# Kernel tuning notes

Hardware: AMD Instinct MI355X
Metric: run time of the kernel (lower is better)

Reference implementation:

```python
import jax, jax.numpy as jnp
import numpy as np

B, IN_DIM, HID, LAT, L, K = 65536, 512, 256, 64, 3, 2048


def setup_inputs() -> dict:
    key = jax.random.key(0)
    ks = jax.random.split(key, 10)
    s = 0.05
    return {
        "x": jax.random.normal(ks[0], (B, IN_DIM), jnp.float32),
        "enc_w1": jax.random.normal(ks[1], (IN_DIM, HID), jnp.float32) * s,
        "enc_b1": jnp.zeros((HID,), jnp.float32),
        "enc_w2": jax.random.normal(ks[2], (HID, LAT), jnp.float32) * s,
        "enc_b2": jnp.zeros((LAT,), jnp.float32),
        "codebooks": jax.random.normal(ks[3], (L, K, LAT), jnp.float32),
        "dec_w1": jax.random.normal(ks[4], (LAT, HID), jnp.float32) * s,
        "dec_b1": jnp.zeros((HID,), jnp.float32),
        "dec_w2": jax.random.normal(ks[5], (HID, IN_DIM), jnp.float32) * s,
        "dec_b2": jnp.zeros((IN_DIM,), jnp.float32),
    }


def reference(x, enc_w1, enc_b1, enc_w2, enc_b2, codebooks,
              dec_w1, dec_b1, dec_w2, dec_b2):
    # encoder: Linear -> ReLU -> Linear
    z = jax.nn.relu(x @ enc_w1 + enc_b1) @ enc_w2 + enc_b2  # [B, LAT]

    quantized = jnp.zeros_like(z)
    codes, residuals = [], []
    num_layers = codebooks.shape[0]
    for i in range(num_layers):  # small fixed layer loop (structurally sequential)
        residual = z - jax.lax.stop_gradient(quantized)  # [B, LAT]
        residuals.append(residual)
        C = codebooks[i]  # [K, LAT]
        # squared euclidean distances (argmin identical to cdist argmin)
        sqdist = (jnp.sum(residual * residual, axis=-1, keepdims=True)
                  - 2.0 * (residual @ C.T)
                  + jnp.sum(C * C, axis=-1))  # [B, K]
        code = jnp.argmin(sqdist, axis=-1)  # [B]
        codes.append(code)
        quantized = C[code] + jax.lax.stop_gradient(quantized)

    # decoder: Linear -> ReLU -> Linear
    x_recon = jax.nn.relu(quantized @ dec_w1 + dec_b1) @ dec_w2 + dec_b2  # [B, IN_DIM]
    return (jnp.stack(codes), x_recon, quantized, jnp.stack(residuals))
```

## Files before the change

### kernel.cpp

```cpp
#include <hip/hip_runtime.h>
#include <float.h>

#define NB      65536
#define IN_DIM  512
#define HID     256
#define LAT     64
#define NLAYERS 3
#define NK      2048
#define DELTA   1e-2f

typedef __attribute__((ext_vector_type(8)))  short s16x8;
typedef __attribute__((ext_vector_type(16))) float fp32x16;

__device__ __forceinline__ unsigned short f2bf(float v) {
  unsigned u = __float_as_uint(v);
  unsigned r = (u + 0x7fffu + ((u >> 16) & 1u)) >> 16;
  return (unsigned short)r;
}
__device__ __forceinline__ float bf2f(unsigned short h) {
  return __uint_as_float((unsigned)h << 16);
}

template<bool RELU>
__global__ __launch_bounds__(256) void gemm_f32(
    const float* __restrict__ A, const float* __restrict__ W,
    const float* __restrict__ bias, float* __restrict__ C,
    int M, int N, int K) {
  __shared__ float As[32][132];
  __shared__ float Bs[32][64];
  const int tid = threadIdx.x;
  const int cg  = tid & 15;
  const int rg  = tid >> 4;
  const int m0  = blockIdx.x * 128;
  const int n0  = blockIdx.y * 64;

  float acc[8][4];
#pragma unroll
  for (int i = 0; i < 8; ++i)
#pragma unroll
    for (int j = 0; j < 4; ++j) acc[i][j] = 0.f;

  for (int k0 = 0; k0 < K; k0 += 32) {
#pragma unroll
    for (int p = 0; p < 4; ++p) {
      int a = tid + p * 256;
      int row = a >> 3, kq = (a & 7) * 4;
      float4 v = *reinterpret_cast<const float4*>(&A[(size_t)(m0 + row) * K + k0 + kq]);
      As[kq + 0][row] = v.x; As[kq + 1][row] = v.y;
      As[kq + 2][row] = v.z; As[kq + 3][row] = v.w;
    }
#pragma unroll
    for (int p = 0; p < 2; ++p) {
      int a = tid + p * 256;
      int kk = a >> 4, nq = (a & 15) * 4;
      *reinterpret_cast<float4*>(&Bs[kk][nq]) =
          *reinterpret_cast<const float4*>(&W[(size_t)(k0 + kk) * N + n0 + nq]);
    }
    __syncthreads();
#pragma unroll
    for (int kk = 0; kk < 32; ++kk) {
      float4 a0 = *reinterpret_cast<const float4*>(&As[kk][rg * 8]);
      float4 a1 = *reinterpret_cast<const float4*>(&As[kk][rg * 8 + 4]);
      float4 b0 = *reinterpret_cast<const float4*>(&Bs[kk][cg * 4]);
      float av[8] = {a0.x, a0.y, a0.z, a0.w, a1.x, a1.y, a1.z, a1.w};
      float bv[4] = {b0.x, b0.y, b0.z, b0.w};
#pragma unroll
      for (int i = 0; i < 8; ++i)
#pragma unroll
        for (int j = 0; j < 4; ++j)
          acc[i][j] = fmaf(av[i], bv[j], acc[i][j]);
    }
    __syncthreads();
  }

  float4 bb = *reinterpret_cast<const float4*>(&bias[n0 + cg * 4]);
  float bv[4] = {bb.x, bb.y, bb.z, bb.w};
#pragma unroll
  for (int i = 0; i < 8; ++i) {
    float vals[4];
#pragma unroll
    for (int j = 0; j < 4; ++j) {
      float v = __fadd_rn(acc[i][j], bv[j]);
      if (RELU) v = fmaxf(v, 0.f);
      vals[j] = v;
    }
    float4 o; o.x = vals[0]; o.y = vals[1]; o.z = vals[2]; o.w = vals[3];
    *reinterpret_cast<float4*>(&C[(size_t)(m0 + rg * 8 + i) * N + n0 + cg * 4]) = o;
  }
}

template<bool RELU>
__global__ __launch_bounds__(256) void gemm128(
    const float* __restrict__ A, const float* __restrict__ W,
    const float* __restrict__ bias, float* __restrict__ C,
    int M, int N, int K) {
  __shared__ float As[16][132];
  __shared__ float Bs[16][132];
  const int tid  = threadIdx.x;
  const int cg   = tid & 15;
  const int rg   = tid >> 4;
  const int sw   = (cg >> 2) & 1;
  const int colA = cg * 8 + sw * 4;
  const int colB = cg * 8 + (sw ^ 1) * 4;
  const int m0   = blockIdx.x * 128;
  const int n0   = blockIdx.y * 128;

  const int arow = tid >> 2;
  const int akq  = (tid & 3) * 4;
  const int bk   = tid >> 5;
  const int bn   = (tid & 31) * 4;

  const float* Ap0 = A + (size_t)(m0 + arow) * K + akq;
  const float* Ap1 = A + (size_t)(m0 + arow + 64) * K + akq;
  const float* Wp0 = W + (size_t)bk * N + n0 + bn;
  const float* Wp1 = W + (size_t)(bk + 8) * N + n0 + bn;

  float acc[8][8];
#pragma unroll
  for (int i = 0; i < 8; ++i)
#pragma unroll
    for (int j = 0; j < 8; ++j) acc[i][j] = 0.f;

  float4 av0, av1, bv0, bv1;
  av0 = *reinterpret_cast<const float4*>(Ap0);
  av1 = *reinterpret_cast<const float4*>(Ap1);
  bv0 = *reinterpret_cast<const float4*>(Wp0);
  bv1 = *reinterpret_cast<const float4*>(Wp1);

  auto write_tile = [&]() {
    As[akq + 0][arow] = av0.x; As[akq + 1][arow] = av0.y;
    As[akq + 2][arow] = av0.z; As[akq + 3][arow] = av0.w;
    As[akq + 0][arow + 64] = av1.x; As[akq + 1][arow + 64] = av1.y;
    As[akq + 2][arow + 64] = av1.z; As[akq + 3][arow + 64] = av1.w;
    *reinterpret_cast<float4*>(&Bs[bk][bn])     = bv0;
    *reinterpret_cast<float4*>(&Bs[bk + 8][bn]) = bv1;
  };
  auto compute_tile = [&]() {
#pragma unroll
    for (int kk = 0; kk < 16; ++kk) {
      float4 a0 = *reinterpret_cast<const float4*>(&As[kk][rg * 8]);
      float4 a1 = *reinterpret_cast<const float4*>(&As[kk][rg * 8 + 4]);
      float4 b0 = *reinterpret_cast<const float4*>(&Bs[kk][colA]);
      float4 b1 = *reinterpret_cast<const float4*>(&Bs[kk][colB]);
      float rv[8] = {a0.x, a0.y, a0.z, a0.w, a1.x, a1.y, a1.z, a1.w};
      float cv[8] = {b0.x, b0.y, b0.z, b0.w, b1.x, b1.y, b1.z, b1.w};
#pragma unroll
      for (int i = 0; i < 8; ++i)
#pragma unroll
        for (int j = 0; j < 8; ++j)
          acc[i][j] = fmaf(rv[i], cv[j], acc[i][j]);
    }
  };

  write_tile();
  __syncthreads();
#pragma unroll 1
  for (int k0 = 16; k0 < K; k0 += 16) {
    av0 = *reinterpret_cast<const float4*>(Ap0 + k0);
    av1 = *reinterpret_cast<const float4*>(Ap1 + k0);
    bv0 = *reinterpret_cast<const float4*>(Wp0 + (size_t)k0 * N);
    bv1 = *reinterpret_cast<const float4*>(Wp1 + (size_t)k0 * N);
    compute_tile();
    __syncthreads();
    write_tile();
    __syncthreads();
  }
  compute_tile();

  float4 bA = *reinterpret_cast<const float4*>(&bias[n0 + colA]);
  float4 bB = *reinterpret_cast<const float4*>(&bias[n0 + colB]);
  float ba[8] = {bA.x, bA.y, bA.z, bA.w, bB.x, bB.y, bB.z, bB.w};
#pragma unroll
  for (int i = 0; i < 8; ++i) {
    size_t row = (size_t)(m0 + rg * 8 + i);
    float o[8];
#pragma unroll
    for (int j = 0; j < 8; ++j) {
      float v = __fadd_rn(acc[i][j], ba[j]);
      if (RELU) v = fmaxf(v, 0.f);
      o[j] = v;
    }
    float4 oA; oA.x = o[0]; oA.y = o[1]; oA.z = o[2]; oA.w = o[3];
    float4 oB; oB.x = o[4]; oB.y = o[5]; oB.z = o[6]; oB.w = o[7];
    *reinterpret_cast<float4*>(&C[row * N + n0 + colA]) = oA;
    *reinterpret_cast<float4*>(&C[row * N + n0 + colB]) = oB;
  }
}

__global__ void cnorm_f32(const float* __restrict__ cb, float* __restrict__ cn) {
  int i = blockIdx.x * blockDim.x + threadIdx.x;
  if (i >= NLAYERS * NK) return;
  const float* row = cb + (size_t)i * LAT;
  float r[8];
#pragma unroll
  for (int j = 0; j < 8; ++j) r[j] = 0.f;
#pragma unroll
  for (int t = 0; t < 8; ++t)
#pragma unroll
    for (int j = 0; j < 8; ++j) {
      float v = row[t * 8 + j];
      r[j] = __fadd_rn(r[j], __fmul_rn(v, v));
    }
  cn[i] = __fadd_rn(__fadd_rn(__fadd_rn(r[0], r[1]), __fadd_rn(r[2], r[3])),
                    __fadd_rn(__fadd_rn(r[4], r[5]), __fadd_rn(r[6], r[7])));
}

__global__ void split_cb(const float* __restrict__ cb,
                         unsigned short* __restrict__ cbf) {
  const int sid  = blockIdx.x * 256 + threadIdx.x;
  const int lane = sid & 63;
  const int grp  = sid >> 6;
  const int fg   = grp & 7;
  const int chl  = grp >> 3;
  const int nt = fg >> 2, ks = fg & 3;
  const int layer = chl >> 5, ch = chl & 31;
  const int code = ch * 64 + nt * 32 + (lane & 31);
  const int k0 = ks * 16 + (lane >> 5) * 8;
  const float* src = cb + ((size_t)layer * NK + code) * LAT + k0;
  float4 a = *(const float4*)src;
  float4 b = *(const float4*)(src + 4);
  float v[8] = {a.x, a.y, a.z, a.w, b.x, b.y, b.z, b.w};
  s16x8 hi, lo;
#pragma unroll
  for (int i = 0; i < 8; ++i) {
    unsigned short h = f2bf(v[i]);
    hi[i] = (short)h;
    lo[i] = (short)f2bf(__fsub_rn(v[i], bf2f(h)));
  }
  *(s16x8*)(cbf + ((size_t)grp * 2 + 0) * 512 + lane * 8) = hi;
  *(s16x8*)(cbf + ((size_t)grp * 2 + 1) * 512 + lane * 8) = lo;
}

__global__ __launch_bounds__(256, 2) void rq_mfma(
    const float* __restrict__ zg,
    const float* __restrict__ cb,
    const unsigned short* __restrict__ cbf,
    const float* __restrict__ cnorm,
    float* __restrict__ out_codes,
    float* __restrict__ out_quant,
    float* __restrict__ out_res) {
  __shared__ float m1S[128][2];
  __shared__ int   candS[128][8];
  __shared__ int   cntS[128][2];
  __shared__ int   flagS[128][2];
  __shared__ int   selS[128];
  __shared__ float rnS[128];
  __shared__ float bestD[256];
  __shared__ int   bestK[256];

  const int tid   = threadIdx.x;
  const int w     = tid >> 6;
  const int rgrp  = w >> 1;
  const int chalf = w & 1;
  const int lane  = tid & 63;
  const int half  = lane >> 5;
  const int lcol  = lane & 31;
  const int rb0   = blockIdx.x * 128;

  s16x8 ah[2][4], al[2][4];

  for (int layer = 0; layer < NLAYERS; ++layer) {
    const float* cbL = cb + (size_t)layer * NK * LAT;
    const float* cnL = cnorm + (size_t)layer * NK;
    const unsigned short* cbfL = cbf + (size_t)layer * (NK * LAT * 2);
    float* resL = out_res + (size_t)layer * NB * LAT;

#pragma unroll
    for (int m = 0; m < 2; ++m) {
      const size_t row = (size_t)(rb0 + rgrp * 64 + m * 32 + lcol);
#pragma unroll
      for (int ks = 0; ks < 4; ++ks) {
        const int k0 = ks * 16 + half * 8;
        const float* zp = zg + row * LAT + k0;
        float4 a = *(const float4*)zp;
        float4 b = *(const float4*)(zp + 4);
        float r[8] = {a.x, a.y, a.z, a.w, b.x, b.y, b.z, b.w};
        if (layer > 0) {
          const float* qp = out_quant + row * LAT + k0;
          float4 qa = *(const float4*)qp;
          float4 qb = *(const float4*)(qp + 4);
          float q[8] = {qa.x, qa.y, qa.z, qa.w, qb.x, qb.y, qb.z, qb.w};
#pragma unroll
          for (int i = 0; i < 8; ++i) r[i] = __fsub_rn(r[i], q[i]);
          if (chalf == 0) {
            float4 o0 = {r[0], r[1], r[2], r[3]};
            float4 o1 = {r[4], r[5], r[6], r[7]};
            *(float4*)(resL + row * LAT + k0) = o0;
            *(float4*)(resL + row * LAT + k0 + 4) = o1;
          }
        }
#pragma unroll
        for (int i = 0; i < 8; ++i) {
          unsigned short hh = f2bf(r[i]);
          float hf = bf2f(hh);
          ah[m][ks][i] = (short)hh;
          al[m][ks][i] = (short)f2bf(__fsub_rn(r[i], hf));
        }
      }
    }
    __syncthreads();

    if (tid < 128) {
      const float* rp = resL + (size_t)(rb0 + tid) * LAT;
      float r8[8] = {0.f, 0.f, 0.f, 0.f, 0.f, 0.f, 0.f, 0.f};
#pragma unroll
      for (int tb = 0; tb < 8; ++tb) {
        float4 x0 = *(const float4*)(rp + tb * 8);
        float4 x1 = *(const float4*)(rp + tb * 8 + 4);
        float v[8] = {x0.x, x0.y, x0.z, x0.w, x1.x, x1.y, x1.z, x1.w};
#pragma unroll
        for (int j = 0; j < 8; ++j)
          r8[j] = __fadd_rn(r8[j], __fmul_rn(v[j], v[j]));
      }
      rnS[tid] = __fadd_rn(
          __fadd_rn(__fadd_rn(r8[0], r8[1]), __fadd_rn(r8[2], r8[3])),
          __fadd_rn(__fadd_rn(r8[4], r8[5]), __fadd_rn(r8[6], r8[7])));
    }

    float v1[2][16], v2[2][16];
    int   i1[2][16];
#pragma unroll
    for (int m = 0; m < 2; ++m)
#pragma unroll
      for (int r = 0; r < 16; ++r) {
        v1[m][r] = FLT_MAX; v2[m][r] = FLT_MAX; i1[m][r] = 0;
      }

#pragma unroll 1
    for (int ch = 0; ch < 16; ++ch) {
      const int chg = chalf * 16 + ch;
      const unsigned short* cf = cbfL + (size_t)chg * 8192;
#pragma unroll
      for (int nt = 0; nt < 2; ++nt) {
        const int kbase = chg * 64 + nt * 32 + lcol;
        float cnv = cnL[kbase];
        s16x8 bh[4], bl[4];
#pragma unroll
        for (int ks = 0; ks < 4; ++ks) {
          bh[ks] = *(const s16x8*)(cf + ((size_t)((nt * 4 + ks) * 2 + 0) * 64 + lane) * 8);
          bl[ks] = *(const s16x8*)(cf + ((size_t)((nt * 4 + ks) * 2 + 1) * 64 + lane) * 8);
        }
        fp32x16 acc0, acc1;
#pragma unroll
        for (int r = 0; r < 16; ++r) { acc0[r] = 0.f; acc1[r] = 0.f; }
#pragma unroll
        for (int ks = 0; ks < 4; ++ks) {
          acc0 = __builtin_amdgcn_mfma_f32_32x32x16_bf16(ah[0][ks], bh[ks], acc0, 0, 0, 0);
          acc1 = __builtin_amdgcn_mfma_f32_32x32x16_bf16(ah[1][ks], bh[ks], acc1, 0, 0, 0);
          acc0 = __builtin_amdgcn_mfma_f32_32x32x16_bf16(ah[0][ks], bl[ks], acc0, 0, 0, 0);
          acc1 = __builtin_amdgcn_mfma_f32_32x32x16_bf16(ah[1][ks], bl[ks], acc1, 0, 0, 0);
          acc0 = __builtin_amdgcn_mfma_f32_32x32x16_bf16(al[0][ks], bh[ks], acc0, 0, 0, 0);
          acc1 = __builtin_amdgcn_mfma_f32_32x32x16_bf16(al[1][ks], bh[ks], acc1, 0, 0, 0);
        }
#pragma unroll
        for (int r = 0; r < 16; ++r) {
          float d0 = fmaf(-2.f, acc0[r], cnv);
          bool c0 = d0 < v1[0][r];
          v2[0][r] = c0 ? v1[0][r] : fminf(v2[0][r], d0);
          v1[0][r] = c0 ? d0 : v1[0][r];
          i1[0][r] = c0 ? kbase : i1[0][r];
          float d1 = fmaf(-2.f, acc1[r], cnv);
          bool c1 = d1 < v1[1][r];
          v2[1][r] = c1 ? v1[1][r] : fminf(v2[1][r], d1);
          v1[1][r] = c1 ? d1 : v1[1][r];
          i1[1][r] = c1 ? kbase : i1[1][r];
        }
      }
    }

#pragma unroll
    for (int m = 0; m < 2; ++m)
#pragma unroll
      for (int r = 0; r < 16; ++r) {
        float m1 = v1[m][r];
        m1 = fminf(m1, __shfl_xor(m1, 1));
        m1 = fminf(m1, __shfl_xor(m1, 2));
        m1 = fminf(m1, __shfl_xor(m1, 4));
        m1 = fminf(m1, __shfl_xor(m1, 8));
        m1 = fminf(m1, __shfl_xor(m1, 16));
        const int rowloc = rgrp * 64 + m * 32 + (r & 3) + 8 * (r >> 2) + 4 * half;
        if (lcol == 0) m1S[rowloc][chalf] = m1;
      }
    __syncthreads();
#pragma unroll
    for (int m = 0; m < 2; ++m)
#pragma unroll
      for (int r = 0; r < 16; ++r) {
        const int rowloc = rgrp * 64 + m * 32 + (r & 3) + 8 * (r >> 2) + 4 * half;
        float thr = fminf(m1S[rowloc][0], m1S[rowloc][1]) + DELTA;
        unsigned long long bc = __ballot(v1[m][r] <= thr);
        unsigned long long bf = __ballot(v2[m][r] <= thr);
        unsigned mc = (unsigned)(bc >> (half * 32));
        unsigned mf = (unsigned)(bf >> (half * 32));
        int pos = __popc(mc & ((1u << lcol) - 1u));
        if (v1[m][r] <= thr && pos < 4) candS[rowloc][chalf * 4 + pos] = i1[m][r];
        if (lcol == 0) {
          int c = __popc(mc);
          cntS[rowloc][chalf]  = (c < 4) ? c : 4;
          flagS[rowloc][chalf] = (mf != 0u) || (c > 4);
        }
      }
    __syncthreads();

    if (tid < 128) {
      const int t = tid;
      if ((flagS[t][0] | flagS[t][1]) == 0) {
        const float* rp = resL + (size_t)(rb0 + t) * LAT;
        float rr[64];
#pragma unroll
        for (int j = 0; j < 16; ++j) {
          float4 x = *(const float4*)(rp + j * 4);
          rr[j * 4 + 0] = x.x; rr[j * 4 + 1] = x.y;
          rr[j * 4 + 2] = x.z; rr[j * 4 + 3] = x.w;
        }
        const float rn = rnS[t];
        float bd = FLT_MAX; int bk = 0x7fffffff;
        const int c0 = cntS[t][0], c1n = cntS[t][1];
        for (int c = 0; c < c0 + c1n; ++c) {
          int k = candS[t][(c < c0) ? c : (4 + c - c0)];
          const float* cp = cbL + (size_t)k * LAT;
          float dot = 0.f;
#pragma unroll
          for (int j = 0; j < 64; ++j) dot = fmaf(rr[j], cp[j], dot);
          float d = __fadd_rn(__fsub_rn(rn, __fmul_rn(2.f, dot)), cnL[k]);
          if (d < bd || (d == bd && k < bk)) { bd = d; bk = k; }
        }
        selS[t] = bk;
        out_codes[(size_t)layer * NB + rb0 + t] = (float)bk;
      }
    }
    __syncthreads();

#pragma unroll 1
    for (int t2 = 0; t2 < 128; ++t2) {
      if ((flagS[t2][0] | flagS[t2][1]) == 0) continue;
      const float* rp = resL + (size_t)(rb0 + t2) * LAT;
      const float rn = rnS[t2];
      float bd = FLT_MAX; int bk = 0x7fffffff;
#pragma unroll 1
      for (int j = 0; j < 8; ++j) {
        int k = tid * 8 + j;
        const float* cp = cbL + (size_t)k * LAT;
        float dot = 0.f;
        for (int q = 0; q < 64; ++q) dot = fmaf(rp[q], cp[q], dot);
        float d = __fadd_rn(__fsub_rn(rn, __fmul_rn(2.f, dot)), cnL[k]);
        if (d < bd || (d == bd && k < bk)) { bd = d; bk = k; }
      }
      bestD[tid] = bd; bestK[tid] = bk;
      __syncthreads();
      if (tid == 0) {
        float gd = FLT_MAX; int gk = 0x7fffffff;
        for (int i = 0; i < 256; ++i) {
          float d = bestD[i]; int k = bestK[i];
          if (d < gd || (d == gd && k < gk)) { gd = d; gk = k; }
        }
        selS[t2] = gk;
        out_codes[(size_t)layer * NB + rb0 + t2] = (float)gk;
      }
      __syncthreads();
    }

    if (chalf == 0) {
#pragma unroll
      for (int m = 0; m < 2; ++m) {
        const int rowloc = rgrp * 64 + m * 32 + lcol;
        const size_t row = (size_t)(rb0 + rowloc);
        const int sel = selS[rowloc];
        const float* cp = cbL + (size_t)sel * LAT;
#pragma unroll
        for (int ks = 0; ks < 4; ++ks) {
          const int k0 = ks * 16 + half * 8;
          float4 c0 = *(const float4*)(cp + k0);
          float4 c1 = *(const float4*)(cp + k0 + 4);
          float* qp = out_quant + row * LAT + k0;
          if (layer == 0) {
            *(float4*)qp = c0; *(float4*)(qp + 4) = c1;
          } else {
            float4 q0 = *(const float4*)qp;
            float4 q1 = *(const float4*)(qp + 4);
            q0.x = __fadd_rn(c0.x, q0.x); q0.y = __fadd_rn(c0.y, q0.y);
            q0.z = __fadd_rn(c0.z, q0.z); q0.w = __fadd_rn(c0.w, q0.w);
            q1.x = __fadd_rn(c1.x, q1.x); q1.y = __fadd_rn(c1.y, q1.y);
            q1.z = __fadd_rn(c1.z, q1.z); q1.w = __fadd_rn(c1.w, q1.w);
            *(float4*)qp = q0; *(float4*)(qp + 4) = q1;
          }
        }
      }
    }
    __syncthreads();
  }
}

extern "C" void kernel_launch(void* const* d_in, const int* in_sizes, int n_in,
                              void* d_out, int out_size, void* d_ws, size_t ws_size,
                              hipStream_t stream) {
  (void)in_sizes; (void)n_in; (void)out_size; (void)ws_size;
  const float* x   = (const float*)d_in[0];
  const float* ew1 = (const float*)d_in[1];
  const float* eb1 = (const float*)d_in[2];
  const float* ew2 = (const float*)d_in[3];
  const float* eb2 = (const float*)d_in[4];
  const float* cbk = (const float*)d_in[5];
  const float* dw1 = (const float*)d_in[6];
  const float* db1 = (const float*)d_in[7];
  const float* dw2 = (const float*)d_in[8];
  const float* db2 = (const float*)d_in[9];

  float* out     = (float*)d_out;
  float* o_codes = out;
  float* o_xrec  = out + (size_t)NLAYERS * NB;
  float* o_quant = o_xrec + (size_t)NB * IN_DIM;
  float* o_res   = o_quant + (size_t)NB * LAT;

  float* h  = (float*)d_ws;
  float* cn = h + (size_t)NB * HID;
  unsigned short* cbf = (unsigned short*)(o_xrec + (size_t)16 * 1024 * 1024);

  cnorm_f32<<<(NLAYERS * NK + 255) / 256, 256, 0, stream>>>(cbk, cn);
  split_cb<<<192, 256, 0, stream>>>(cbk, cbf);
  gemm128<true ><<<dim3(NB / 128, HID / 128),    256, 0, stream>>>(x, ew1, eb1, h,     NB, HID,    IN_DIM);
  gemm_f32<false><<<dim3(NB / 128, LAT / 64),    256, 0, stream>>>(h, ew2, eb2, o_res, NB, LAT,    HID);
  rq_mfma<<<NB / 128, 256, 0, stream>>>(o_res, cbk, cbf, cn, o_codes, o_quant, o_res);
  gemm128<true ><<<dim3(NB / 128, HID / 128),    256, 0, stream>>>(o_quant, dw1, db1, h,      NB, HID,    LAT);
  gemm128<false><<<dim3(NB / 128, IN_DIM / 128), 256, 0, stream>>>(h,       dw2, db2, o_xrec, NB, IN_DIM, HID);
}
```

Before: 825.2 us.

## Use split-bf16 MFMA decoder GEMMs and split RQ codebook scan across four waves

Adds split_w to pre-split the decoder weights into bf16 hi/lo MFMA fragments. It replaces the decoder's FP32 gemm128 calls with dec1/dec2 kernels that use 3-pass bf16 MFMA, storing the hidden activations as bf16 hi/lo pairs. The RQ kernel now handles 64 rows per block, with each of the four waves scanning a quarter of the codebook, which doubles the grid. The top-2 update is rewritten with min/max instead of selects. The split-bf16 path adds error versus FP32 and depends on the workspace being large enough, otherwise it falls back to the old path.

```diff
diff --git a/kernel.cpp b/kernel.cpp
--- a/kernel.cpp
+++ b/kernel.cpp
@@ -231,6 +231,30 @@
   *(s16x8*)(cbf + ((size_t)grp * 2 + 1) * 512 + lane * 8) = lo;
 }
 
+__global__ void split_w(const float* __restrict__ W,
+                        unsigned short* __restrict__ wf, int K, int N) {
+  const int total = (K / 16) * (N / 32) * 64;
+  const int idx = blockIdx.x * 256 + threadIdx.x;
+  if (idx >= total) return;
+  const int lane = idx & 63;
+  const int grp  = idx >> 6;
+  const int ntn  = N / 32;
+  const int ks   = grp / ntn;
+  const int ntg  = grp % ntn;
+  const int col  = ntg * 32 + (lane & 31);
+  const int k0   = ks * 16 + (lane >> 5) * 8;
+  s16x8 hi, lo;
+#pragma unroll
+  for (int i = 0; i < 8; ++i) {
+    float v = W[(size_t)(k0 + i) * N + col];
+    unsigned short h = f2bf(v);
+    hi[i] = (short)h;
+    lo[i] = (short)f2bf(__fsub_rn(v, bf2f(h)));
+  }
+  *(s16x8*)(wf + ((size_t)grp * 2 + 0) * 512 + lane * 8) = hi;
+  *(s16x8*)(wf + ((size_t)grp * 2 + 1) * 512 + lane * 8) = lo;
+}
+
 __global__ __launch_bounds__(256, 2) void rq_mfma(
     const float* __restrict__ zg,
     const float* __restrict__ cb,
@@ -239,23 +263,21 @@
     float* __restrict__ out_codes,
     float* __restrict__ out_quant,
     float* __restrict__ out_res) {
-  __shared__ float m1S[128][2];
-  __shared__ int   candS[128][8];
-  __shared__ int   cntS[128][2];
-  __shared__ int   flagS[128][2];
-  __shared__ int   selS[128];
-  __shared__ float rnS[128];
+  __shared__ float m1S[64][4];
+  __shared__ int   candS[64][16];
+  __shared__ int   cntS[64][4];
+  __shared__ int   flagS[64][4];
+  __shared__ int   selS[64];
+  __shared__ float rnS[64];
   __shared__ float bestD[256];
   __shared__ int   bestK[256];
 
-  const int tid   = threadIdx.x;
-  const int w     = tid >> 6;
-  const int rgrp  = w >> 1;
-  const int chalf = w & 1;
-  const int lane  = tid & 63;
-  const int half  = lane >> 5;
-  const int lcol  = lane & 31;
-  const int rb0   = blockIdx.x * 128;
+  const int tid  = threadIdx.x;
+  const int w    = tid >> 6;
+  const int lane = tid & 63;
+  const int half = lane >> 5;
+  const int lcol = lane & 31;
+  const int rb0  = blockIdx.x * 64;
 
   s16x8 ah[2][4], al[2][4];
 
@@ -267,7 +289,7 @@
 
 #pragma unroll
     for (int m = 0; m < 2; ++m) {
-      const size_t row = (size_t)(rb0 + rgrp * 64 + m * 32 + lcol);
+      const size_t row = (size_t)(rb0 + m * 32 + lcol);
 #pragma unroll
       for (int ks = 0; ks < 4; ++ks) {
         const int k0 = ks * 16 + half * 8;
@@ -282,7 +304,7 @@
           float q[8] = {qa.x, qa.y, qa.z, qa.w, qb.x, qb.y, qb.z, qb.w};
 #pragma unroll
           for (int i = 0; i < 8; ++i) r[i] = __fsub_rn(r[i], q[i]);
-          if (chalf == 0) {
+          if (w == 0) {
             float4 o0 = {r[0], r[1], r[2], r[3]};
             float4 o1 = {r[4], r[5], r[6], r[7]};
             *(float4*)(resL + row * LAT + k0) = o0;
@@ -300,7 +322,7 @@
     }
     __syncthreads();
 
-    if (tid < 128) {
+    if (tid < 64) {
       const float* rp = resL + (size_t)(rb0 + tid) * LAT;
       float r8[8] = {0.f, 0.f, 0.f, 0.f, 0.f, 0.f, 0.f, 0.f};
 #pragma unroll
@@ -327,8 +349,8 @@
       }
 
 #pragma unroll 1
-    for (int ch = 0; ch < 16; ++ch) {
-      const int chg = chalf * 16 + ch;
+    for (int ch = 0; ch < 8; ++ch) {
+      const int chg = w * 8 + ch;
       const unsigned short* cf = cbfL + (size_t)chg * 8192;
 #pragma unroll
       for (int nt = 0; nt < 2; ++nt) {
@@ -354,16 +376,22 @@
         }
 #pragma unroll
         for (int r = 0; r < 16; ++r) {
-          float d0 = fmaf(-2.f, acc0[r], cnv);
-          bool c0 = d0 < v1[0][r];
-          v2[0][r] = c0 ? v1[0][r] : fminf(v2[0][r], d0);
-          v1[0][r] = c0 ? d0 : v1[0][r];
-          i1[0][r] = c0 ? kbase : i1[0][r];
-          float d1 = fmaf(-2.f, acc1[r], cnv);
-          bool c1 = d1 < v1[1][r];
-          v2[1][r] = c1 ? v1[1][r] : fminf(v2[1][r], d1);
-          v1[1][r] = c1 ? d1 : v1[1][r];
-          i1[1][r] = c1 ? kbase : i1[1][r];
+          {
+            float d = fmaf(-2.f, acc0[r], cnv);
+            float t = fmaxf(d, v1[0][r]);
+            v2[0][r] = fminf(v2[0][r], t);
+            bool c = d < v1[0][r];
+            i1[0][r] = c ? kbase : i1[0][r];
+            v1[0][r] = fminf(v1[0][r], d);
+          }
+          {
+            float d = fmaf(-2.f, acc1[r], cnv);
+            float t = fmaxf(d, v1[1][r]);
+            v2[1][r] = fminf(v2[1][r], t);
+            bool c = d < v1[1][r];
+            i1[1][r] = c ? kbase : i1[1][r];
+            v1[1][r] = fminf(v1[1][r], d);
+          }
         }
       }
     }
@@ -378,33 +406,34 @@
         m1 = fminf(m1, __shfl_xor(m1, 4));
         m1 = fminf(m1, __shfl_xor(m1, 8));
         m1 = fminf(m1, __shfl_xor(m1, 16));
-        const int rowloc = rgrp * 64 + m * 32 + (r & 3) + 8 * (r >> 2) + 4 * half;
-        if (lcol == 0) m1S[rowloc][chalf] = m1;
+        const int rowloc = m * 32 + (r & 3) + 8 * (r >> 2) + 4 * half;
+        if (lcol == 0) m1S[rowloc][w] = m1;
       }
     __syncthreads();
 #pragma unroll
     for (int m = 0; m < 2; ++m)
 #pragma unroll
       for (int r = 0; r < 16; ++r) {
-        const int rowloc = rgrp * 64 + m * 32 + (r & 3) + 8 * (r >> 2) + 4 * half;
-        float thr = fminf(m1S[rowloc][0], m1S[rowloc][1]) + DELTA;
+        const int rowloc = m * 32 + (r & 3) + 8 * (r >> 2) + 4 * half;
+        float thr = fminf(fminf(m1S[rowloc][0], m1S[rowloc][1]),
+                          fminf(m1S[rowloc][2], m1S[rowloc][3])) + DELTA;
         unsigned long long bc = __ballot(v1[m][r] <= thr);
         unsigned long long bf = __ballot(v2[m][r] <= thr);
         unsigned mc = (unsigned)(bc >> (half * 32));
         unsigned mf = (unsigned)(bf >> (half * 32));
         int pos = __popc(mc & ((1u << lcol) - 1u));
-        if (v1[m][r] <= thr && pos < 4) candS[rowloc][chalf * 4 + pos] = i1[m][r];
+        if (v1[m][r] <= thr && pos < 4) candS[rowloc][w * 4 + pos] = i1[m][r];
         if (lcol == 0) {
           int c = __popc(mc);
-          cntS[rowloc][chalf]  = (c < 4) ? c : 4;
-          flagS[rowloc][chalf] = (mf != 0u) || (c > 4);
-        }
-      }
-    __syncthreads();
-
-    if (tid < 128) {
+          cntS[rowloc][w]  = (c < 4) ? c : 4;
+          flagS[rowloc][w] = (mf != 0u) || (c > 4);
+        }
+      }
+    __syncthreads();
+
+    if (tid < 64) {
       const int t = tid;
-      if ((flagS[t][0] | flagS[t][1]) == 0) {
+      if ((flagS[t][0] | flagS[t][1] | flagS[t][2] | flagS[t][3]) == 0) {
         const float* rp = resL + (size_t)(rb0 + t) * LAT;
         float rr[64];
 #pragma unroll
@@ -415,15 +444,18 @@
         }
         const float rn = rnS[t];
         float bd = FLT_MAX; int bk = 0x7fffffff;
-        const int c0 = cntS[t][0], c1n = cntS[t][1];
-        for (int c = 0; c < c0 + c1n; ++c) {
-          int k = candS[t][(c < c0) ? c : (4 + c - c0)];
-          const float* cp = cbL + (size_t)k * LAT;
-          float dot = 0.f;
-#pragma unroll
-          for (int j = 0; j < 64; ++j) dot = fmaf(rr[j], cp[j], dot);
-          float d = __fadd_rn(__fsub_rn(rn, __fmul_rn(2.f, dot)), cnL[k]);
-          if (d < bd || (d == bd && k < bk)) { bd = d; bk = k; }
+#pragma unroll 1
+        for (int w4 = 0; w4 < 4; ++w4) {
+          const int cc = cntS[t][w4];
+          for (int c = 0; c < cc; ++c) {
+            int k = candS[t][w4 * 4 + c];
+            const float* cp = cbL + (size_t)k * LAT;
+            float dot = 0.f;
+#pragma unroll
+            for (int j = 0; j < 64; ++j) dot = fmaf(rr[j], cp[j], dot);
+            float d = __fadd_rn(__fsub_rn(rn, __fmul_rn(2.f, dot)), cnL[k]);
+            if (d < bd || (d == bd && k < bk)) { bd = d; bk = k; }
+          }
         }
         selS[t] = bk;
         out_codes[(size_t)layer * NB + rb0 + t] = (float)bk;
@@ -432,8 +464,8 @@
     __syncthreads();
 
 #pragma unroll 1
-    for (int t2 = 0; t2 < 128; ++t2) {
-      if ((flagS[t2][0] | flagS[t2][1]) == 0) continue;
+    for (int t2 = 0; t2 < 64; ++t2) {
+      if ((flagS[t2][0] | flagS[t2][1] | flagS[t2][2] | flagS[t2][3]) == 0) continue;
       const float* rp = resL + (size_t)(rb0 + t2) * LAT;
       const float rn = rnS[t2];
       float bd = FLT_MAX; int bk = 0x7fffffff;
@@ -460,41 +492,148 @@
       __syncthreads();
     }
 
-    if (chalf == 0) {
-#pragma unroll
-      for (int m = 0; m < 2; ++m) {
-        const int rowloc = rgrp * 64 + m * 32 + lcol;
-        const size_t row = (size_t)(rb0 + rowloc);
-        const int sel = selS[rowloc];
-        const float* cp = cbL + (size_t)sel * LAT;
-#pragma unroll
-        for (int ks = 0; ks < 4; ++ks) {
-          const int k0 = ks * 16 + half * 8;
-          float4 c0 = *(const float4*)(cp + k0);
-          float4 c1 = *(const float4*)(cp + k0 + 4);
-          float* qp = out_quant + row * LAT + k0;
-          if (layer == 0) {
-            *(float4*)qp = c0; *(float4*)(qp + 4) = c1;
-          } else {
-            float4 q0 = *(const float4*)qp;
-            float4 q1 = *(const float4*)(qp + 4);
-            q0.x = __fadd_rn(c0.x, q0.x); q0.y = __fadd_rn(c0.y, q0.y);
-            q0.z = __fadd_rn(c0.z, q0.z); q0.w = __fadd_rn(c0.w, q0.w);
-            q1.x = __fadd_rn(c1.x, q1.x); q1.y = __fadd_rn(c1.y, q1.y);
-            q1.z = __fadd_rn(c1.z, q1.z); q1.w = __fadd_rn(c1.w, q1.w);
-            *(float4*)qp = q0; *(float4*)(qp + 4) = q1;
-          }
-        }
-      }
-    }
-    __syncthreads();
+    if (w < 2) {
+      const int m = w;
+      const int rowloc = m * 32 + lcol;
+      const size_t row = (size_t)(rb0 + rowloc);
+      const int sel = selS[rowloc];
+      const float* cp = cbL + (size_t)sel * LAT;
+#pragma unroll
+      for (int ks = 0; ks < 4; ++ks) {
+        const int k0 = ks * 16 + half * 8;
+        float4 c0 = *(const float4*)(cp + k0);
+        float4 c1 = *(const float4*)(cp + k0 + 4);
+        float* qp = out_quant + row * LAT + k0;
+        if (layer == 0) {
+          *(float4*)qp = c0; *(float4*)(qp + 4) = c1;
+        } else {
+          float4 q0 = *(const float4*)qp;
+          float4 q1 = *(const float4*)(qp + 4);
+          q0.x = __fadd_rn(c0.x, q0.x); q0.y = __fadd_rn(c0.y, q0.y);
+          q0.z = __fadd_rn(c0.z, q0.z); q0.w = __fadd_rn(c0.w, q0.w);
+          q1.x = __fadd_rn(c1.x, q1.x); q1.y = __fadd_rn(c1.y, q1.y);
+          q1.z = __fadd_rn(c1.z, q1.z); q1.w = __fadd_rn(c1.w, q1.w);
+          *(float4*)qp = q0; *(float4*)(qp + 4) = q1;
+        }
+      }
+    }
+    __syncthreads();
+  }
+}
+
+__global__ __launch_bounds__(256) void dec1_mfma(
+    const float* __restrict__ q, const unsigned short* __restrict__ wf,
+    const float* __restrict__ bias,
+    unsigned short* __restrict__ h_hi, unsigned short* __restrict__ h_lo) {
+  const int tid  = threadIdx.x;
+  const int w    = tid >> 6;
+  const int lane = tid & 63;
+  const int half = lane >> 5;
+  const int lcol = lane & 31;
+  const int m0   = blockIdx.x * 128 + w * 32;
+  const int n0   = blockIdx.y * 128;
+
+  fp32x16 acc[4];
+#pragma unroll
+  for (int nt = 0; nt < 4; ++nt)
+#pragma unroll
+    for (int r = 0; r < 16; ++r) acc[nt][r] = 0.f;
+
+  const size_t arow = (size_t)(m0 + lcol);
+#pragma unroll
+  for (int ks = 0; ks < 4; ++ks) {
+    const float* ap = q + arow * LAT + ks * 16 + half * 8;
+    float4 a0 = *(const float4*)ap;
+    float4 a1 = *(const float4*)(ap + 4);
+    float av[8] = {a0.x, a0.y, a0.z, a0.w, a1.x, a1.y, a1.z, a1.w};
+    s16x8 ah, al;
+#pragma unroll
+    for (int i = 0; i < 8; ++i) {
+      unsigned short hh = f2bf(av[i]);
+      ah[i] = (short)hh;
+      al[i] = (short)f2bf(__fsub_rn(av[i], bf2f(hh)));
+    }
+#pragma unroll
+    for (int nt = 0; nt < 4; ++nt) {
+      const int grp = ks * 8 + (blockIdx.y * 4 + nt);
+      const unsigned short* base = wf + (size_t)grp * 1024;
+      s16x8 bh = *(const s16x8*)(base + lane * 8);
+      s16x8 bl = *(const s16x8*)(base + 512 + lane * 8);
+      acc[nt] = __builtin_amdgcn_mfma_f32_32x32x16_bf16(ah, bh, acc[nt], 0, 0, 0);
+      acc[nt] = __builtin_amdgcn_mfma_f32_32x32x16_bf16(ah, bl, acc[nt], 0, 0, 0);
+      acc[nt] = __builtin_amdgcn_mfma_f32_32x32x16_bf16(al, bh, acc[nt], 0, 0, 0);
+    }
+  }
+
+#pragma unroll
+  for (int nt = 0; nt < 4; ++nt) {
+    const int col = n0 + nt * 32 + lcol;
+    const float b = bias[col];
+#pragma unroll
+    for (int r = 0; r < 16; ++r) {
+      const int rowo = (r & 3) + 8 * (r >> 2) + 4 * half;
+      const size_t grow = (size_t)(m0 + rowo);
+      float v = fmaxf(__fadd_rn(acc[nt][r], b), 0.f);
+      unsigned short hh = f2bf(v);
+      h_hi[grow * HID + col] = hh;
+      h_lo[grow * HID + col] = f2bf(__fsub_rn(v, bf2f(hh)));
+    }
+  }
+}
+
+__global__ __launch_bounds__(256) void dec2_mfma(
+    const unsigned short* __restrict__ h_hi,
+    const unsigned short* __restrict__ h_lo,
+    const unsigned short* __restrict__ wf,
+    const float* __restrict__ bias, float* __restrict__ C) {
+  const int tid  = threadIdx.x;
+  const int w    = tid >> 6;
+  const int lane = tid & 63;
+  const int half = lane >> 5;
+  const int lcol = lane & 31;
+  const int m0   = blockIdx.x * 128 + w * 32;
+  const int n0   = blockIdx.y * 128;
+
+  fp32x16 acc[4];
+#pragma unroll
+  for (int nt = 0; nt < 4; ++nt)
+#pragma unroll
+    for (int r = 0; r < 16; ++r) acc[nt][r] = 0.f;
+
+  const size_t arow = (size_t)(m0 + lcol);
+#pragma unroll 1
+  for (int ks = 0; ks < 16; ++ks) {
+    const size_t aoff = arow * HID + ks * 16 + half * 8;
+    s16x8 ah = *(const s16x8*)(h_hi + aoff);
+    s16x8 al = *(const s16x8*)(h_lo + aoff);
+#pragma unroll
+    for (int nt = 0; nt < 4; ++nt) {
+      const int grp = ks * 16 + (blockIdx.y * 4 + nt);
+      const unsigned short* base = wf + (size_t)grp * 1024;
+      s16x8 bh = *(const s16x8*)(base + lane * 8);
+      s16x8 bl = *(const s16x8*)(base + 512 + lane * 8);
+      acc[nt] = __builtin_amdgcn_mfma_f32_32x32x16_bf16(ah, bh, acc[nt], 0, 0, 0);
+      acc[nt] = __builtin_amdgcn_mfma_f32_32x32x16_bf16(ah, bl, acc[nt], 0, 0, 0);
+      acc[nt] = __builtin_amdgcn_mfma_f32_32x32x16_bf16(al, bh, acc[nt], 0, 0, 0);
+    }
+  }
+
+#pragma unroll
+  for (int nt = 0; nt < 4; ++nt) {
+    const int col = n0 + nt * 32 + lcol;
+    const float b = bias[col];
+#pragma unroll
+    for (int r = 0; r < 16; ++r) {
+      const int rowo = (r & 3) + 8 * (r >> 2) + 4 * half;
+      C[(size_t)(m0 + rowo) * IN_DIM + col] = __fadd_rn(acc[nt][r], b);
+    }
   }
 }
 
 extern "C" void kernel_launch(void* const* d_in, const int* in_sizes, int n_in,
                               void* d_out, int out_size, void* d_ws, size_t ws_size,
                               hipStream_t stream) {
-  (void)in_sizes; (void)n_in; (void)out_size; (void)ws_size;
+  (void)in_sizes; (void)n_in; (void)out_size;
   const float* x   = (const float*)d_in[0];
   const float* ew1 = (const float*)d_in[1];
   const float* eb1 = (const float*)d_in[2];
@@ -512,15 +651,32 @@
   float* o_quant = o_xrec + (size_t)NB * IN_DIM;
   float* o_res   = o_quant + (size_t)NB * LAT;
 
-  float* h  = (float*)d_ws;
-  float* cn = h + (size_t)NB * HID;
+  char* ws = (char*)d_ws;
+  float* h            = (float*)ws;
+  unsigned short* hhi = (unsigned short*)ws;
+  unsigned short* hlo = (unsigned short*)(ws + (size_t)32 * 1024 * 1024);
+  float* cn           = (float*)(ws + (size_t)64 * 1024 * 1024);
+  unsigned short* w1f = (unsigned short*)(ws + (size_t)64 * 1024 * 1024 + 32768);
+  unsigned short* w2f = (unsigned short*)(ws + (size_t)64 * 1024 * 1024 + 32768 + 65536);
+  const size_t ws_need = (size_t)64 * 1024 * 1024 + 32768 + 65536 + 524288;
+  const bool fast_dec = ws_size >= ws_need;
+
   unsigned short* cbf = (unsigned short*)(o_xrec + (size_t)16 * 1024 * 1024);
 
   cnorm_f32<<<(NLAYERS * NK + 255) / 256, 256, 0, stream>>>(cbk, cn);
   split_cb<<<192, 256, 0, stream>>>(cbk, cbf);
-  gemm128<true ><<<dim3(NB / 128, HID / 128),    256, 0, stream>>>(x, ew1, eb1, h,     NB, HID,    IN_DIM);
-  gemm_f32<false><<<dim3(NB / 128, LAT / 64),    256, 0, stream>>>(h, ew2, eb2, o_res, NB, LAT,    HID);
-  rq_mfma<<<NB / 128, 256, 0, stream>>>(o_res, cbk, cbf, cn, o_codes, o_quant, o_res);
-  gemm128<true ><<<dim3(NB / 128, HID / 128),    256, 0, stream>>>(o_quant, dw1, db1, h,      NB, HID,    LAT);
-  gemm128<false><<<dim3(NB / 128, IN_DIM / 128), 256, 0, stream>>>(h,       dw2, db2, o_xrec, NB, IN_DIM, HID);
-}
+  if (fast_dec) {
+    split_w<<<((LAT / 16) * (HID / 32) * 64 + 255) / 256, 256, 0, stream>>>(dw1, w1f, LAT, HID);
+    split_w<<<((HID / 16) * (IN_DIM / 32) * 64 + 255) / 256, 256, 0, stream>>>(dw2, w2f, HID, IN_DIM);
+  }
+  gemm128<true ><<<dim3(NB / 128, HID / 128), 256, 0, stream>>>(x, ew1, eb1, h,     NB, HID, IN_DIM);
+  gemm_f32<false><<<dim3(NB / 128, LAT / 64),  256, 0, stream>>>(h, ew2, eb2, o_res, NB, LAT, HID);
+  rq_mfma<<<NB / 64, 256, 0, stream>>>(o_res, cbk, cbf, cn, o_codes, o_quant, o_res);
+  if (fast_dec) {
+    dec1_mfma<<<dim3(NB / 128, 2), 256, 0, stream>>>(o_quant, w1f, db1, hhi, hlo);
+    dec2_mfma<<<dim3(NB / 128, 4), 256, 0, stream>>>(hhi, hlo, w2f, db2, o_xrec);
+  } else {
+    gemm128<true ><<<dim3(NB / 128, HID / 128),    256, 0, stream>>>(o_quant, dw1, db1, h,      NB, HID,    LAT);
+    gemm128<false><<<dim3(NB / 128, IN_DIM / 128), 256, 0, stream>>>(h,       dw2, db2, o_xrec, NB, IN_DIM, HID);
+  }
+}
```

Result: faster. 800.3 us (-3.0%).
